# Kernel optimization log

Measured on AMD Instinct MI355X. Metric: run time of the kernel, lower is better.

The kernel has to match this reference:

```python
import jax, jax.numpy as jnp
import numpy as np

D_MODEL = 1024
NUM_HEADS = 16
D_K = D_MODEL // NUM_HEADS
THETA = 10000.0
BATCH = 2
SEQ = 2048


def _trunc_normal(key, shape, std):
    # approximate trunc_normal init; exact init distribution is irrelevant for correctness
    return jnp.clip(jax.random.normal(key, shape) * std, -3.0 * std, 3.0 * std)


def setup_inputs() -> dict:
    key = jax.random.key(0)
    ks = jax.random.split(key, 6)
    std = np.sqrt(2.0 / (D_MODEL + D_MODEL)).astype(np.float32)
    x = jax.random.normal(ks[0], (BATCH, SEQ, D_MODEL), dtype=jnp.float32)
    token_positions = jnp.tile(jnp.arange(SEQ, dtype=jnp.int32), (BATCH, 1))
    wq = _trunc_normal(ks[1], (D_MODEL, D_MODEL), std)  # (out, in)
    wk = _trunc_normal(ks[2], (D_MODEL, D_MODEL), std)
    wv = _trunc_normal(ks[3], (D_MODEL, D_MODEL), std)
    wo = _trunc_normal(ks[4], (D_MODEL, D_MODEL), std)
    return {"in_features": x, "wq": wq, "wk": wk, "wv": wv, "wo": wo,
            "token_positions": token_positions}


def _apply_rope(x, token_positions):
    # x: (B, H, S, d_k); token_positions: (B, S)
    half = D_K // 2
    inv_freq = 1.0 / (THETA ** (2.0 * jnp.arange(half, dtype=jnp.float32) / D_K))
    ang = token_positions.astype(jnp.float32)[..., None] * inv_freq  # (B, S, half)
    cos = jnp.cos(ang)[:, None, :, :]  # (B, 1, S, half) broadcast over heads
    sin = jnp.sin(ang)[:, None, :, :]
    x_even = x[..., 0::2]
    x_odd = x[..., 1::2]
    rot_even = x_even * cos - x_odd * sin
    rot_odd = x_even * sin + x_odd * cos
    return jnp.stack([rot_even, rot_odd], axis=-1).reshape(x.shape)


def reference(in_features, wq, wk, wv, wo, token_positions):
    B, S, _ = in_features.shape
    # bias-free linear: weight is (out, in)
    q = jnp.einsum('bsi,oi->bso', in_features, wq)
    k = jnp.einsum('bsi,oi->bso', in_features, wk)
    v = jnp.einsum('bsi,oi->bso', in_features, wv)
    # split heads: (B, H, S, d_k)
    def split(t):
        return t.reshape(B, S, NUM_HEADS, D_K).transpose(0, 2, 1, 3)
    qh, kh, vh = split(q), split(k), split(v)
    qh = _apply_rope(qh, token_positions)
    kh = _apply_rope(kh, token_positions)
    scale = 1.0 / jnp.sqrt(jnp.float32(D_K))
    logits = jnp.einsum('bhqd,bhkd->bhqk', qh, kh) * scale  # (B, H, S, S)
    causal = jnp.tril(jnp.ones((S, S), dtype=bool))
    logits = jnp.where(causal, logits, -jnp.inf)
    weights = jax.nn.softmax(logits, axis=-1)
    out = jnp.einsum('bhqk,bhkd->bhqd', weights, vh)  # (B, H, S, d_k)
    out = out.transpose(0, 2, 1, 3).reshape(B, S, D_MODEL)
    return jnp.einsum('bsi,oi->bso', out, wo)
```

## Files before the change

### kernel.cpp

```cpp
#include <hip/hip_runtime.h>
#include <hip/hip_bf16.h>
#include <math.h>

#define D_MODEL 1024
#define NUM_HEADS 16
#define DK 64
#define BATCH 2
#define SEQ 2048
#define NROWS (BATCH * SEQ)

typedef __bf16 bf16x8 __attribute__((ext_vector_type(8)));
typedef __bf16 bf16x4 __attribute__((ext_vector_type(4)));
typedef float f32x4 __attribute__((ext_vector_type(4)));

#define GLOAD_LDS16(g, l)                                          \
  __builtin_amdgcn_global_load_lds(                                \
      (const __attribute__((address_space(1))) void*)(g),          \
      (__attribute__((address_space(3))) void*)(l), 16, 0, 0)

#define LDS_FENCE() asm volatile("s_waitcnt lgkmcnt(0)" ::: "memory")

__global__ void cvt_all_kernel(const float* __restrict__ x,
                               const float* __restrict__ wq,
                               const float* __restrict__ wk,
                               const float* __restrict__ wv,
                               const float* __restrict__ wo,
                               __hip_bfloat16* __restrict__ xb,
                               __hip_bfloat16* __restrict__ wqkvb,
                               __hip_bfloat16* __restrict__ wob) {
  int t = blockIdx.x * 256 + threadIdx.x;
  const float* src;
  __hip_bfloat16* dst;
  int off;
  if (t < 1048576) {
    src = x; dst = xb; off = t;
  } else {
    int u = t - 1048576;
    int w = u >> 18;
    off = u & 262143;
    src = (w == 0) ? wq : (w == 1) ? wk : (w == 2) ? wv : wo;
    dst = (w < 3) ? (wqkvb + (size_t)w * 1048576) : wob;
  }
  float4 v = reinterpret_cast<const float4*>(src)[off];
  union { __hip_bfloat16 h[4]; uint2 u; } tmp;
  tmp.h[0] = __float2bfloat16(v.x);
  tmp.h[1] = __float2bfloat16(v.y);
  tmp.h[2] = __float2bfloat16(v.z);
  tmp.h[3] = __float2bfloat16(v.w);
  reinterpret_cast<uint2*>(dst)[off] = tmp.u;
}

template <int NSPLIT, bool OUT_F32>
__global__ __launch_bounds__(256)
void gemm_bt_kernel(const __hip_bfloat16* __restrict__ A,
                    const __hip_bfloat16* __restrict__ W,
                    void* __restrict__ O0, void* __restrict__ O1,
                    void* __restrict__ O2) {
  __shared__ __hip_bfloat16 sA[2][128 * 32];
  __shared__ __hip_bfloat16 sB[2][128 * 32];
  const int tid = threadIdx.x;
  const int wave = tid >> 6, lane = tid & 63, quad = lane >> 4, l16 = lane & 15;
  const int wm = (wave >> 1) * 64, wn = (wave & 1) * 64;
  const int bm = blockIdx.x * 128;
  const int bnG = blockIdx.y * 128;
  void* O;
  int ocol;
  if (NSPLIT == 3) {
    int which = blockIdx.y >> 3;
    O = (which == 0) ? O0 : (which == 1) ? O1 : O2;
    ocol = bnG & 1023;
  } else {
    O = O0;
    ocol = bnG;
  }
  const int srow = lane >> 2, scol = (lane & 3) * 8;

#pragma unroll
  for (int c = 0; c < 2; ++c) {
    int ch = wave + c * 4;
    GLOAD_LDS16(&A[(size_t)(bm + ch * 16 + srow) * D_MODEL + scol], &sA[0][ch * 512]);
    GLOAD_LDS16(&W[(size_t)(bnG + ch * 16 + srow) * D_MODEL + scol], &sB[0][ch * 512]);
  }

  f32x4 acc[4][4] = {};
  for (int it = 0; it < 32; ++it) {
    __syncthreads();
    if (it + 1 < 32) {
      const int k0 = (it + 1) * 32, nb = (it + 1) & 1;
#pragma unroll
      for (int c = 0; c < 2; ++c) {
        int ch = wave + c * 4;
        GLOAD_LDS16(&A[(size_t)(bm + ch * 16 + srow) * D_MODEL + k0 + scol],
                    &sA[nb][ch * 512]);
        GLOAD_LDS16(&W[(size_t)(bnG + ch * 16 + srow) * D_MODEL + k0 + scol],
                    &sB[nb][ch * 512]);
      }
    }
    const int cb = it & 1;
    bf16x8 af[4], bfb[4];
#pragma unroll
    for (int i = 0; i < 4; ++i)
      af[i] = *reinterpret_cast<bf16x8*>(&sA[cb][(wm + i * 16 + l16) * 32 + quad * 8]);
#pragma unroll
    for (int j = 0; j < 4; ++j)
      bfb[j] = *reinterpret_cast<bf16x8*>(&sB[cb][(wn + j * 16 + l16) * 32 + quad * 8]);
#pragma unroll
    for (int i = 0; i < 4; ++i)
#pragma unroll
      for (int j = 0; j < 4; ++j)
        acc[i][j] = __builtin_amdgcn_mfma_f32_16x16x32_bf16(af[i], bfb[j], acc[i][j], 0, 0, 0);
  }

#pragma unroll
  for (int i = 0; i < 4; ++i)
#pragma unroll
    for (int j = 0; j < 4; ++j)
#pragma unroll
      for (int r = 0; r < 4; ++r) {
        int row = bm + wm + i * 16 + quad * 4 + r;
        int col = ocol + wn + j * 16 + l16;
        if (OUT_F32)
          reinterpret_cast<float*>(O)[(size_t)row * D_MODEL + col] = acc[i][j][r];
        else
          reinterpret_cast<__hip_bfloat16*>(O)[(size_t)row * D_MODEL + col] =
              __float2bfloat16(acc[i][j][r]);
      }
}

__global__ void rope_kernel(__hip_bfloat16* __restrict__ Q,
                            __hip_bfloat16* __restrict__ K,
                            const int* __restrict__ pos) {
  constexpr float QS = 0.18033688011112042f;
  int t = blockIdx.x * 256 + threadIdx.x;
  int row = t >> 7;
  int c = t & 127;
  int h = c >> 3, co = (c & 7) * 8;
  float ps = (float)pos[row];
  size_t off = (size_t)row * D_MODEL + h * DK + co;
  bf16x8 q = *reinterpret_cast<const bf16x8*>(&Q[off]);
  bf16x8 k = *reinterpret_cast<const bf16x8*>(&K[off]);
#pragma unroll
  for (int j = 0; j < 4; ++j) {
    float p = (float)((co >> 1) + j);
    float ang = ps * exp2f(-p * 0.41524101186091903f);
    float cs = cosf(ang), sn = sinf(ang);
    float qe = (float)q[2 * j], qo = (float)q[2 * j + 1];
    q[2 * j]     = (__bf16)((qe * cs - qo * sn) * QS);
    q[2 * j + 1] = (__bf16)((qe * sn + qo * cs) * QS);
    float ke = (float)k[2 * j], ko = (float)k[2 * j + 1];
    k[2 * j]     = (__bf16)(ke * cs - ko * sn);
    k[2 * j + 1] = (__bf16)(ke * sn + ko * cs);
  }
  *reinterpret_cast<bf16x8*>(&Q[off]) = q;
  *reinterpret_cast<bf16x8*>(&K[off]) = k;
}

__global__ __launch_bounds__(256)
void attn_kernel(const __hip_bfloat16* __restrict__ Q,
                 const __hip_bfloat16* __restrict__ K,
                 const __hip_bfloat16* __restrict__ V,
                 __hip_bfloat16* __restrict__ Ao) {
  constexpr int LS = 66;
  __shared__ __hip_bfloat16 sK[2][64 * LS];
  __shared__ __hip_bfloat16 sVt[2][64 * LS];
  __shared__ __hip_bfloat16 sPt[4][16 * 64];
  const int tid = threadIdx.x;
  const int wave = tid >> 6, lane = tid & 63, quad = lane >> 4, l16 = lane & 15;
  const int idx = blockIdx.x;
  const int qb = 15 - (idx >> 5);
  const int hb = idx & 31;
  const int h = hb & 15, b = hb >> 4;
  const int ho = h * DK;
  const size_t rowbase = (size_t)b * SEQ;
  const int sbs[2] = {qb * 128 + wave * 16, qb * 128 + (7 - wave) * 16};
  const __hip_bfloat16* Kbase = K + rowbase * D_MODEL + ho;
  const unsigned short* Vu =
      reinterpret_cast<const unsigned short*>(V + rowbase * D_MODEL + ho);

  bf16x8 aq[2][2];
#pragma unroll
  for (int s = 0; s < 2; ++s)
#pragma unroll
    for (int kk = 0; kk < 2; ++kk)
      aq[s][kk] = *reinterpret_cast<const bf16x8*>(
          &Q[(rowbase + sbs[s] + l16) * D_MODEL + ho + kk * 32 + quad * 8]);

  f32x4 o_acc[2][4] = {};
  float l_run[2] = {0.f, 0.f};

  const int krow = tid >> 2, kc = (tid & 3) * 16;
  const int vd = lane;

  {
    *reinterpret_cast<bf16x8*>(&sK[0][krow * LS + kc]) =
        *reinterpret_cast<const bf16x8*>(&Kbase[(size_t)krow * D_MODEL + kc]);
    *reinterpret_cast<bf16x8*>(&sK[0][krow * LS + kc + 8]) =
        *reinterpret_cast<const bf16x8*>(&Kbase[(size_t)krow * D_MODEL + kc + 8]);
#pragma unroll
    for (int i = 0; i < 8; ++i) {
      int kvp = wave * 8 + i;
      unsigned lo = Vu[(size_t)(2 * kvp) * D_MODEL + vd];
      unsigned hi = Vu[(size_t)(2 * kvp + 1) * D_MODEL + vd];
      *reinterpret_cast<unsigned*>(&sVt[0][vd * LS + 2 * kvp]) = lo | (hi << 16);
    }
  }

  const int nt = 2 * qb + 2;
  for (int t = 0; t < nt; ++t) {
    __syncthreads();
    const int buf = t & 1;
    const bool hn = (t + 1) < nt;
    bf16x8 kn0, kn1;
    unsigned vw[8];
    if (hn) {
      const int kvn = (t + 1) * 64;
      kn0 = *reinterpret_cast<const bf16x8*>(
          &Kbase[(size_t)(kvn + krow) * D_MODEL + kc]);
      kn1 = *reinterpret_cast<const bf16x8*>(
          &Kbase[(size_t)(kvn + krow) * D_MODEL + kc + 8]);
#pragma unroll
      for (int i = 0; i < 8; ++i) {
        int kvp = wave * 8 + i;
        unsigned lo = Vu[(size_t)(kvn + 2 * kvp) * D_MODEL + vd];
        unsigned hi = Vu[(size_t)(kvn + 2 * kvp + 1) * D_MODEL + vd];
        vw[i] = lo | (hi << 16);
      }
    }

    const int kv0 = t * 64;
    bf16x8 ak[2][4], bv[2][4];
#pragma unroll
    for (int kk = 0; kk < 2; ++kk)
#pragma unroll
      for (int j = 0; j < 4; ++j) {
        ak[kk][j] = *reinterpret_cast<bf16x8*>(
            &sK[buf][(j * 16 + l16) * LS + kk * 32 + quad * 8]);
        bv[kk][j] = *reinterpret_cast<bf16x8*>(
            &sVt[buf][(j * 16 + l16) * LS + kk * 32 + quad * 8]);
      }

#pragma unroll
    for (int s = 0; s < 2; ++s) {
      const int sb = sbs[s];
      if (kv0 > sb + 15) continue;
      f32x4 sv[4] = {};
#pragma unroll
      for (int kk = 0; kk < 2; ++kk)
#pragma unroll
        for (int j = 0; j < 4; ++j)
          sv[j] = __builtin_amdgcn_mfma_f32_16x16x32_bf16(ak[kk][j], aq[s][kk],
                                                          sv[j], 0, 0, 0);
      if (kv0 + 63 > sb) {
#pragma unroll
        for (int j = 0; j < 4; ++j)
#pragma unroll
          for (int r = 0; r < 4; ++r)
            if (kv0 + j * 16 + quad * 4 + r > sb + l16) sv[j][r] = -INFINITY;
      }
      float ls = 0.f;
#pragma unroll
      for (int j = 0; j < 4; ++j) {
        bf16x4 pk;
#pragma unroll
        for (int r = 0; r < 4; ++r) {
          float p = __builtin_amdgcn_exp2f(sv[j][r]);
          ls += p;
          pk[r] = (__bf16)p;
        }
        int wgr = (2 * j + (quad >> 1)) ^ (l16 & 7);
        *reinterpret_cast<bf16x4*>(
            &sPt[wave][l16 * 64 + wgr * 8 + (quad & 1) * 4]) = pk;
      }
      l_run[s] += ls;
      LDS_FENCE();
#pragma unroll
      for (int kk = 0; kk < 2; ++kk) {
        int rgr = (4 * kk + quad) ^ (l16 & 7);
        bf16x8 ap = *reinterpret_cast<bf16x8*>(&sPt[wave][l16 * 64 + rgr * 8]);
#pragma unroll
        for (int jd = 0; jd < 4; ++jd)
          o_acc[s][jd] = __builtin_amdgcn_mfma_f32_16x16x32_bf16(
              ap, bv[kk][jd], o_acc[s][jd], 0, 0, 0);
      }
    }

    if (hn) {
      const int nb = buf ^ 1;
      *reinterpret_cast<bf16x8*>(&sK[nb][krow * LS + kc]) = kn0;
      *reinterpret_cast<bf16x8*>(&sK[nb][krow * LS + kc + 8]) = kn1;
#pragma unroll
      for (int i = 0; i < 8; ++i) {
        int kvp = wave * 8 + i;
        *reinterpret_cast<unsigned*>(&sVt[nb][vd * LS + 2 * kvp]) = vw[i];
      }
    }
  }

#pragma unroll
  for (int s = 0; s < 2; ++s) {
    float l = l_run[s];
    l += __shfl_xor(l, 16);
    l += __shfl_xor(l, 32);
    __hip_bfloat16* Aobase = Ao + (rowbase + sbs[s]) * D_MODEL + ho;
#pragma unroll
    for (int r = 0; r < 4; ++r) {
      float linv = 1.0f / __shfl(l, quad * 4 + r);
#pragma unroll
      for (int jd = 0; jd < 4; ++jd)
        Aobase[(size_t)(quad * 4 + r) * D_MODEL + jd * 16 + l16] =
            __float2bfloat16(o_acc[s][jd][r] * linv);
    }
  }
}

extern "C" void kernel_launch(void* const* d_in, const int* in_sizes, int n_in,
                              void* d_out, int out_size, void* d_ws, size_t ws_size,
                              hipStream_t stream) {
  const float* x = (const float*)d_in[0];
  const float* wq = (const float*)d_in[1];
  const float* wk = (const float*)d_in[2];
  const float* wv = (const float*)d_in[3];
  const float* wo = (const float*)d_in[4];
  const int* tpos = (const int*)d_in[5];
  float* out = (float*)d_out;
  char* ws = (char*)d_ws;

  __hip_bfloat16* xb    = (__hip_bfloat16*)(ws);
  __hip_bfloat16* wqkvb = (__hip_bfloat16*)(ws + (size_t)(8)  * 1048576);
  __hip_bfloat16* wob   = (__hip_bfloat16*)(ws + (size_t)(14) * 1048576);
  __hip_bfloat16* Qb    = (__hip_bfloat16*)(ws + (size_t)(16) * 1048576);
  __hip_bfloat16* Kb    = (__hip_bfloat16*)(ws + (size_t)(24) * 1048576);
  __hip_bfloat16* Vb    = (__hip_bfloat16*)(ws + (size_t)(32) * 1048576);
  __hip_bfloat16* Aob   = xb;

  cvt_all_kernel<<<8192, 256, 0, stream>>>(x, wq, wk, wv, wo, xb, wqkvb, wob);

  gemm_bt_kernel<3, false><<<dim3(32, 24), 256, 0, stream>>>(
      xb, wqkvb, Qb, Kb, Vb);

  rope_kernel<<<2048, 256, 0, stream>>>(Qb, Kb, tpos);

  attn_kernel<<<512, 256, 0, stream>>>(Qb, Kb, Vb, Aob);

  gemm_bt_kernel<1, true><<<dim3(32, 8), 256, 0, stream>>>(
      Aob, wob, out, out, out);
}
```

Before: 217.7 us.

## Fuse RoPE into attention, pair causal query blocks, retile output GEMM

```diff
diff --git a/kernel.cpp b/kernel.cpp
--- a/kernel.cpp
+++ b/kernel.cpp
@@ -19,6 +19,18 @@
       (__attribute__((address_space(3))) void*)(l), 16, 0, 0)
 
 #define LDS_FENCE() asm volatile("s_waitcnt lgkmcnt(0)" ::: "memory")
+
+__device__ inline bf16x8 rope8(bf16x8 v, float pos, int p0, float scale) {
+#pragma unroll
+  for (int j = 0; j < 4; ++j) {
+    float ang = pos * exp2f(-(float)(p0 + j) * 0.41524101186091903f);
+    float cs = cosf(ang), sn = sinf(ang);
+    float e = (float)v[2 * j], o = (float)v[2 * j + 1];
+    v[2 * j]     = (__bf16)((e * cs - o * sn) * scale);
+    v[2 * j + 1] = (__bf16)((e * sn + o * cs) * scale);
+  }
+  return v;
+}
 
 __global__ void cvt_all_kernel(const float* __restrict__ x,
                                const float* __restrict__ wq,
@@ -50,12 +62,12 @@
   reinterpret_cast<uint2*>(dst)[off] = tmp.u;
 }
 
-template <int NSPLIT, bool OUT_F32>
 __global__ __launch_bounds__(256)
-void gemm_bt_kernel(const __hip_bfloat16* __restrict__ A,
-                    const __hip_bfloat16* __restrict__ W,
-                    void* __restrict__ O0, void* __restrict__ O1,
-                    void* __restrict__ O2) {
+void gemm_qkv_kernel(const __hip_bfloat16* __restrict__ A,
+                     const __hip_bfloat16* __restrict__ W,
+                     __hip_bfloat16* __restrict__ O0,
+                     __hip_bfloat16* __restrict__ O1,
+                     __hip_bfloat16* __restrict__ O2) {
   __shared__ __hip_bfloat16 sA[2][128 * 32];
   __shared__ __hip_bfloat16 sB[2][128 * 32];
   const int tid = threadIdx.x;
@@ -63,16 +75,9 @@
   const int wm = (wave >> 1) * 64, wn = (wave & 1) * 64;
   const int bm = blockIdx.x * 128;
   const int bnG = blockIdx.y * 128;
-  void* O;
-  int ocol;
-  if (NSPLIT == 3) {
-    int which = blockIdx.y >> 3;
-    O = (which == 0) ? O0 : (which == 1) ? O1 : O2;
-    ocol = bnG & 1023;
-  } else {
-    O = O0;
-    ocol = bnG;
-  }
+  int which = blockIdx.y >> 3;
+  __hip_bfloat16* O = (which == 0) ? O0 : (which == 1) ? O1 : O2;
+  const int ocol = bnG & 1023;
   const int srow = lane >> 2, scol = (lane & 3) * 8;
 
 #pragma unroll
@@ -119,47 +124,77 @@
       for (int r = 0; r < 4; ++r) {
         int row = bm + wm + i * 16 + quad * 4 + r;
         int col = ocol + wn + j * 16 + l16;
-        if (OUT_F32)
-          reinterpret_cast<float*>(O)[(size_t)row * D_MODEL + col] = acc[i][j][r];
-        else
-          reinterpret_cast<__hip_bfloat16*>(O)[(size_t)row * D_MODEL + col] =
-              __float2bfloat16(acc[i][j][r]);
-      }
-}
-
-__global__ void rope_kernel(__hip_bfloat16* __restrict__ Q,
-                            __hip_bfloat16* __restrict__ K,
-                            const int* __restrict__ pos) {
-  constexpr float QS = 0.18033688011112042f;
-  int t = blockIdx.x * 256 + threadIdx.x;
-  int row = t >> 7;
-  int c = t & 127;
-  int h = c >> 3, co = (c & 7) * 8;
-  float ps = (float)pos[row];
-  size_t off = (size_t)row * D_MODEL + h * DK + co;
-  bf16x8 q = *reinterpret_cast<const bf16x8*>(&Q[off]);
-  bf16x8 k = *reinterpret_cast<const bf16x8*>(&K[off]);
-#pragma unroll
-  for (int j = 0; j < 4; ++j) {
-    float p = (float)((co >> 1) + j);
-    float ang = ps * exp2f(-p * 0.41524101186091903f);
-    float cs = cosf(ang), sn = sinf(ang);
-    float qe = (float)q[2 * j], qo = (float)q[2 * j + 1];
-    q[2 * j]     = (__bf16)((qe * cs - qo * sn) * QS);
-    q[2 * j + 1] = (__bf16)((qe * sn + qo * cs) * QS);
-    float ke = (float)k[2 * j], ko = (float)k[2 * j + 1];
-    k[2 * j]     = (__bf16)(ke * cs - ko * sn);
-    k[2 * j + 1] = (__bf16)(ke * sn + ko * cs);
-  }
-  *reinterpret_cast<bf16x8*>(&Q[off]) = q;
-  *reinterpret_cast<bf16x8*>(&K[off]) = k;
+        O[(size_t)row * D_MODEL + col] = __float2bfloat16(acc[i][j][r]);
+      }
+}
+
+__global__ __launch_bounds__(256)
+void gemm_out_kernel(const __hip_bfloat16* __restrict__ A,
+                     const __hip_bfloat16* __restrict__ W,
+                     float* __restrict__ O) {
+  __shared__ __hip_bfloat16 sA[2][64 * 32];
+  __shared__ __hip_bfloat16 sB[2][128 * 32];
+  const int tid = threadIdx.x;
+  const int wave = tid >> 6, lane = tid & 63, quad = lane >> 4, l16 = lane & 15;
+  const int mh = (wave >> 1) * 32, nh = (wave & 1) * 64;
+  const int bm = blockIdx.x * 64, bn = blockIdx.y * 128;
+  const int srow = lane >> 2, scol = (lane & 3) * 8;
+
+  GLOAD_LDS16(&A[(size_t)(bm + wave * 16 + srow) * D_MODEL + scol], &sA[0][wave * 512]);
+#pragma unroll
+  for (int c = 0; c < 2; ++c) {
+    int ch = wave + c * 4;
+    GLOAD_LDS16(&W[(size_t)(bn + ch * 16 + srow) * D_MODEL + scol], &sB[0][ch * 512]);
+  }
+
+  f32x4 acc[2][4] = {};
+  for (int it = 0; it < 32; ++it) {
+    __syncthreads();
+    if (it + 1 < 32) {
+      const int k0 = (it + 1) * 32, nb = (it + 1) & 1;
+      GLOAD_LDS16(&A[(size_t)(bm + wave * 16 + srow) * D_MODEL + k0 + scol],
+                  &sA[nb][wave * 512]);
+#pragma unroll
+      for (int c = 0; c < 2; ++c) {
+        int ch = wave + c * 4;
+        GLOAD_LDS16(&W[(size_t)(bn + ch * 16 + srow) * D_MODEL + k0 + scol],
+                    &sB[nb][ch * 512]);
+      }
+    }
+    const int cb = it & 1;
+    bf16x8 af[2], bfb[4];
+#pragma unroll
+    for (int i = 0; i < 2; ++i)
+      af[i] = *reinterpret_cast<bf16x8*>(&sA[cb][(mh + i * 16 + l16) * 32 + quad * 8]);
+#pragma unroll
+    for (int j = 0; j < 4; ++j)
+      bfb[j] = *reinterpret_cast<bf16x8*>(&sB[cb][(nh + j * 16 + l16) * 32 + quad * 8]);
+#pragma unroll
+    for (int i = 0; i < 2; ++i)
+#pragma unroll
+      for (int j = 0; j < 4; ++j)
+        acc[i][j] = __builtin_amdgcn_mfma_f32_16x16x32_bf16(af[i], bfb[j], acc[i][j], 0, 0, 0);
+  }
+
+#pragma unroll
+  for (int i = 0; i < 2; ++i)
+#pragma unroll
+    for (int j = 0; j < 4; ++j)
+#pragma unroll
+      for (int r = 0; r < 4; ++r) {
+        int row = bm + mh + i * 16 + quad * 4 + r;
+        int col = bn + nh + j * 16 + l16;
+        O[(size_t)row * D_MODEL + col] = acc[i][j][r];
+      }
 }
 
 __global__ __launch_bounds__(256)
 void attn_kernel(const __hip_bfloat16* __restrict__ Q,
                  const __hip_bfloat16* __restrict__ K,
                  const __hip_bfloat16* __restrict__ V,
+                 const int* __restrict__ tpos,
                  __hip_bfloat16* __restrict__ Ao) {
+  constexpr float QS = 0.18033688011112042f;
   constexpr int LS = 66;
   __shared__ __hip_bfloat16 sK[2][64 * LS];
   __shared__ __hip_bfloat16 sVt[2][64 * LS];
@@ -167,131 +202,148 @@
   const int tid = threadIdx.x;
   const int wave = tid >> 6, lane = tid & 63, quad = lane >> 4, l16 = lane & 15;
   const int idx = blockIdx.x;
-  const int qb = 15 - (idx >> 5);
-  const int hb = idx & 31;
-  const int h = hb & 15, b = hb >> 4;
+  const int bh = idx & 31;
+  const int half = (idx >> 5) & 1;
+  const int pi = idx >> 6;
+  const int qlo = pi, qhi = 15 - pi;
+  const int h = bh & 15, b = bh >> 4;
   const int ho = h * DK;
   const size_t rowbase = (size_t)b * SEQ;
-  const int sbs[2] = {qb * 128 + wave * 16, qb * 128 + (7 - wave) * 16};
+  const int jL = half * 4 + wave, jU = 7 - jL;
+  const int sbs[2] = {qlo * 128 + jL * 16, qhi * 128 + jU * 16};
+  const int nt = ((qhi * 128 + (7 - half * 4) * 16 + 15) >> 6) + 1;
   const __hip_bfloat16* Kbase = K + rowbase * D_MODEL + ho;
   const unsigned short* Vu =
       reinterpret_cast<const unsigned short*>(V + rowbase * D_MODEL + ho);
 
   bf16x8 aq[2][2];
 #pragma unroll
-  for (int s = 0; s < 2; ++s)
-#pragma unroll
-    for (int kk = 0; kk < 2; ++kk)
-      aq[s][kk] = *reinterpret_cast<const bf16x8*>(
+  for (int s = 0; s < 2; ++s) {
+    float posq = (float)tpos[rowbase + sbs[s] + l16];
+#pragma unroll
+    for (int kk = 0; kk < 2; ++kk) {
+      bf16x8 v = *reinterpret_cast<const bf16x8*>(
           &Q[(rowbase + sbs[s] + l16) * D_MODEL + ho + kk * 32 + quad * 8]);
+      aq[s][kk] = rope8(v, posq, kk * 16 + quad * 4, QS);
+    }
+  }
 
   f32x4 o_acc[2][4] = {};
   float l_run[2] = {0.f, 0.f};
 
   const int krow = tid >> 2, kc = (tid & 3) * 16;
+  const int kp0a = kc >> 1, kp0b = (kc + 8) >> 1;
   const int vd = lane;
 
   {
-    *reinterpret_cast<bf16x8*>(&sK[0][krow * LS + kc]) =
-        *reinterpret_cast<const bf16x8*>(&Kbase[(size_t)krow * D_MODEL + kc]);
-    *reinterpret_cast<bf16x8*>(&sK[0][krow * LS + kc + 8]) =
-        *reinterpret_cast<const bf16x8*>(&Kbase[(size_t)krow * D_MODEL + kc + 8]);
-#pragma unroll
-    for (int i = 0; i < 8; ++i) {
-      int kvp = wave * 8 + i;
-      unsigned lo = Vu[(size_t)(2 * kvp) * D_MODEL + vd];
-      unsigned hi = Vu[(size_t)(2 * kvp + 1) * D_MODEL + vd];
-      *reinterpret_cast<unsigned*>(&sVt[0][vd * LS + 2 * kvp]) = lo | (hi << 16);
-    }
-  }
-
-  const int nt = 2 * qb + 2;
+    float posk = (float)tpos[rowbase + krow];
+    bf16x8 k0 = *reinterpret_cast<const bf16x8*>(&Kbase[(size_t)krow * D_MODEL + kc]);
+    bf16x8 k1 = *reinterpret_cast<const bf16x8*>(&Kbase[(size_t)krow * D_MODEL + kc + 8]);
+    *reinterpret_cast<bf16x8*>(&sK[0][krow * LS + kc]) = rope8(k0, posk, kp0a, 1.0f);
+    *reinterpret_cast<bf16x8*>(&sK[0][krow * LS + kc + 8]) = rope8(k1, posk, kp0b, 1.0f);
+#pragma unroll
+    for (int c = 0; c < 8; ++c) {
+      int u = c * 256 + tid;
+      int d = u & 63, kvp = u >> 6;
+      unsigned lo = Vu[(size_t)(2 * kvp) * D_MODEL + d];
+      unsigned hi = Vu[(size_t)(2 * kvp + 1) * D_MODEL + d];
+      *reinterpret_cast<unsigned*>(&sVt[0][d * LS + 2 * kvp]) = lo | (hi << 16);
+    }
+  }
+
   for (int t = 0; t < nt; ++t) {
     __syncthreads();
     const int buf = t & 1;
     const bool hn = (t + 1) < nt;
     bf16x8 kn0, kn1;
+    int posn = 0;
     unsigned vw[8];
     if (hn) {
       const int kvn = (t + 1) * 64;
+      posn = tpos[rowbase + kvn + krow];
       kn0 = *reinterpret_cast<const bf16x8*>(
           &Kbase[(size_t)(kvn + krow) * D_MODEL + kc]);
       kn1 = *reinterpret_cast<const bf16x8*>(
           &Kbase[(size_t)(kvn + krow) * D_MODEL + kc + 8]);
 #pragma unroll
-      for (int i = 0; i < 8; ++i) {
-        int kvp = wave * 8 + i;
-        unsigned lo = Vu[(size_t)(kvn + 2 * kvp) * D_MODEL + vd];
-        unsigned hi = Vu[(size_t)(kvn + 2 * kvp + 1) * D_MODEL + vd];
-        vw[i] = lo | (hi << 16);
+      for (int c = 0; c < 8; ++c) {
+        int u = c * 256 + tid;
+        int d = u & 63, kvp = u >> 6;
+        unsigned lo = Vu[(size_t)(kvn + 2 * kvp) * D_MODEL + d];
+        unsigned hi = Vu[(size_t)(kvn + 2 * kvp + 1) * D_MODEL + d];
+        vw[c] = lo | (hi << 16);
       }
     }
 
     const int kv0 = t * 64;
-    bf16x8 ak[2][4], bv[2][4];
-#pragma unroll
-    for (int kk = 0; kk < 2; ++kk)
-#pragma unroll
-      for (int j = 0; j < 4; ++j) {
-        ak[kk][j] = *reinterpret_cast<bf16x8*>(
-            &sK[buf][(j * 16 + l16) * LS + kk * 32 + quad * 8]);
-        bv[kk][j] = *reinterpret_cast<bf16x8*>(
-            &sVt[buf][(j * 16 + l16) * LS + kk * 32 + quad * 8]);
-      }
-
-#pragma unroll
-    for (int s = 0; s < 2; ++s) {
-      const int sb = sbs[s];
-      if (kv0 > sb + 15) continue;
-      f32x4 sv[4] = {};
+    if (kv0 <= sbs[1] + 15) {
+      bf16x8 ak[2][4], bv[2][4];
 #pragma unroll
       for (int kk = 0; kk < 2; ++kk)
 #pragma unroll
-        for (int j = 0; j < 4; ++j)
-          sv[j] = __builtin_amdgcn_mfma_f32_16x16x32_bf16(ak[kk][j], aq[s][kk],
-                                                          sv[j], 0, 0, 0);
-      if (kv0 + 63 > sb) {
-#pragma unroll
-        for (int j = 0; j < 4; ++j)
-#pragma unroll
-          for (int r = 0; r < 4; ++r)
-            if (kv0 + j * 16 + quad * 4 + r > sb + l16) sv[j][r] = -INFINITY;
-      }
-      float ls = 0.f;
-#pragma unroll
-      for (int j = 0; j < 4; ++j) {
-        bf16x4 pk;
-#pragma unroll
-        for (int r = 0; r < 4; ++r) {
-          float p = __builtin_amdgcn_exp2f(sv[j][r]);
-          ls += p;
-          pk[r] = (__bf16)p;
+        for (int j = 0; j < 4; ++j) {
+          ak[kk][j] = *reinterpret_cast<bf16x8*>(
+              &sK[buf][(j * 16 + l16) * LS + kk * 32 + quad * 8]);
+          bv[kk][j] = *reinterpret_cast<bf16x8*>(
+              &sVt[buf][(j * 16 + l16) * LS + kk * 32 + quad * 8]);
         }
-        int wgr = (2 * j + (quad >> 1)) ^ (l16 & 7);
-        *reinterpret_cast<bf16x4*>(
-            &sPt[wave][l16 * 64 + wgr * 8 + (quad & 1) * 4]) = pk;
-      }
-      l_run[s] += ls;
-      LDS_FENCE();
-#pragma unroll
-      for (int kk = 0; kk < 2; ++kk) {
-        int rgr = (4 * kk + quad) ^ (l16 & 7);
-        bf16x8 ap = *reinterpret_cast<bf16x8*>(&sPt[wave][l16 * 64 + rgr * 8]);
-#pragma unroll
-        for (int jd = 0; jd < 4; ++jd)
-          o_acc[s][jd] = __builtin_amdgcn_mfma_f32_16x16x32_bf16(
-              ap, bv[kk][jd], o_acc[s][jd], 0, 0, 0);
+
+#pragma unroll
+      for (int s = 0; s < 2; ++s) {
+        const int sb = sbs[s];
+        if (kv0 > sb + 15) continue;
+        f32x4 sv[4] = {};
+#pragma unroll
+        for (int kk = 0; kk < 2; ++kk)
+#pragma unroll
+          for (int j = 0; j < 4; ++j)
+            sv[j] = __builtin_amdgcn_mfma_f32_16x16x32_bf16(ak[kk][j], aq[s][kk],
+                                                            sv[j], 0, 0, 0);
+        if (kv0 + 63 > sb) {
+#pragma unroll
+          for (int j = 0; j < 4; ++j)
+#pragma unroll
+            for (int r = 0; r < 4; ++r)
+              if (kv0 + j * 16 + quad * 4 + r > sb + l16) sv[j][r] = -INFINITY;
+        }
+        float ls = 0.f;
+#pragma unroll
+        for (int j = 0; j < 4; ++j) {
+          bf16x4 pk;
+#pragma unroll
+          for (int r = 0; r < 4; ++r) {
+            float p = __builtin_amdgcn_exp2f(sv[j][r]);
+            ls += p;
+            pk[r] = (__bf16)p;
+          }
+          int wgr = (2 * j + (quad >> 1)) ^ (l16 & 7);
+          *reinterpret_cast<bf16x4*>(
+              &sPt[wave][l16 * 64 + wgr * 8 + (quad & 1) * 4]) = pk;
+        }
+        l_run[s] += ls;
+        LDS_FENCE();
+#pragma unroll
+        for (int kk = 0; kk < 2; ++kk) {
+          int rgr = (4 * kk + quad) ^ (l16 & 7);
+          bf16x8 ap = *reinterpret_cast<bf16x8*>(&sPt[wave][l16 * 64 + rgr * 8]);
+#pragma unroll
+          for (int jd = 0; jd < 4; ++jd)
+            o_acc[s][jd] = __builtin_amdgcn_mfma_f32_16x16x32_bf16(
+                ap, bv[kk][jd], o_acc[s][jd], 0, 0, 0);
+        }
       }
     }
 
     if (hn) {
       const int nb = buf ^ 1;
-      *reinterpret_cast<bf16x8*>(&sK[nb][krow * LS + kc]) = kn0;
-      *reinterpret_cast<bf16x8*>(&sK[nb][krow * LS + kc + 8]) = kn1;
-#pragma unroll
-      for (int i = 0; i < 8; ++i) {
-        int kvp = wave * 8 + i;
-        *reinterpret_cast<unsigned*>(&sVt[nb][vd * LS + 2 * kvp]) = vw[i];
+      float pk = (float)posn;
+      *reinterpret_cast<bf16x8*>(&sK[nb][krow * LS + kc]) = rope8(kn0, pk, kp0a, 1.0f);
+      *reinterpret_cast<bf16x8*>(&sK[nb][krow * LS + kc + 8]) = rope8(kn1, pk, kp0b, 1.0f);
+#pragma unroll
+      for (int c = 0; c < 8; ++c) {
+        int u = c * 256 + tid;
+        int d = u & 63, kvp = u >> 6;
+        *reinterpret_cast<unsigned*>(&sVt[nb][d * LS + 2 * kvp]) = vw[c];
       }
     }
   }
@@ -335,13 +387,9 @@
 
   cvt_all_kernel<<<8192, 256, 0, stream>>>(x, wq, wk, wv, wo, xb, wqkvb, wob);
 
-  gemm_bt_kernel<3, false><<<dim3(32, 24), 256, 0, stream>>>(
-      xb, wqkvb, Qb, Kb, Vb);
-
-  rope_kernel<<<2048, 256, 0, stream>>>(Qb, Kb, tpos);
-
-  attn_kernel<<<512, 256, 0, stream>>>(Qb, Kb, Vb, Aob);
-
-  gemm_bt_kernel<1, true><<<dim3(32, 8), 256, 0, stream>>>(
-      Aob, wob, out, out, out);
-}
+  gemm_qkv_kernel<<<dim3(32, 24), 256, 0, stream>>>(xb, wqkvb, Qb, Kb, Vb);
+
+  attn_kernel<<<512, 256, 0, stream>>>(Qb, Kb, Vb, tpos, Aob);
+
+  gemm_out_kernel<<<dim3(64, 8), 256, 0, stream>>>(Aob, wob, out);
+}
```

New measurement: 252.9 us. 16.2% more time.
